# Kernel tuning notes

Hardware: AMD Instinct MI355X
Metric: run time of the kernel (lower is better)

The kernel has to match this reference:

```python
import jax, jax.numpy as jnp
import numpy as np

N_NODES = 50000
N_EDGES = 800000
F_IN, HID, N_CLS = 128, 64, 40


def gcn_conv(x, edge_index, W, b):
    """PyG GCNConv: add self-loops, symmetric normalization, linear, aggregate, bias."""
    n = x.shape[0]
    loop = jnp.arange(n, dtype=edge_index.dtype)
    src = jnp.concatenate([edge_index[0], loop])  # [E+N]
    dst = jnp.concatenate([edge_index[1], loop])  # [E+N]
    deg = jax.ops.segment_sum(jnp.ones_like(dst, dtype=x.dtype), dst, num_segments=n)
    dinv = jnp.where(deg > 0, jax.lax.rsqrt(deg), 0.0)
    norm = dinv[src] * dinv[dst]                   # [E+N]
    h = x @ W                                      # [N, out]
    out = jax.ops.segment_sum(h[src] * norm[:, None], dst, num_segments=n)
    return out + b


def setup_inputs() -> dict:
    key = jax.random.key(0)
    k1, k2, k3, k4 = jax.random.split(key, 4)
    x = jax.random.normal(k1, (N_NODES, F_IN), dtype=jnp.float32)
    edge_index = jax.random.randint(k2, (2, N_EDGES), 0, N_NODES, dtype=jnp.int32)
    W1 = jax.random.normal(k3, (F_IN, HID), dtype=jnp.float32) / np.sqrt(F_IN)
    b1 = jnp.zeros((HID,), dtype=jnp.float32)
    W2 = jax.random.normal(k4, (HID, N_CLS), dtype=jnp.float32) / np.sqrt(HID)
    b2 = jnp.zeros((N_CLS,), dtype=jnp.float32)
    return {"x": x, "edge_index": edge_index, "W1": W1, "b1": b1, "W2": W2, "b2": b2}


def reference(x, edge_index, W1, b1, W2, b2):
    # layer 1: GCNConv -> ReLU -> Dropout(eval = identity)
    h = jax.nn.relu(gcn_conv(x, edge_index, W1, b1))
    # layer 2: GCNConv -> ReLU -> Dropout(eval = identity); return_logits=True
    h = jax.nn.relu(gcn_conv(h, edge_index, W2, b2))
    return h
```

## Files before the change

### kernel.cpp

```cpp
#include <hip/hip_runtime.h>
#include <hip/hip_bf16.h>
#include <hip/hip_fp16.h>


#define N_FEAT_IN 128
#define N_HID 64
#define N_CLS 40
#define CAP 64

__device__ __forceinline__ void h8_acc(uint4 u, float4& a0, float4& a1) {
    __half2* h = (__half2*)&u;
    float2 f0 = __half22float2(h[0]);
    float2 f1 = __half22float2(h[1]);
    float2 f2 = __half22float2(h[2]);
    float2 f3 = __half22float2(h[3]);
    a0.x += f0.x; a0.y += f0.y; a0.z += f1.x; a0.w += f1.y;
    a1.x += f2.x; a1.y += f2.y; a1.z += f3.x; a1.w += f3.y;
}

__device__ __forceinline__ void h8_fma(uint4 u, float w, float4& a0, float4& a1) {
    __half2* h = (__half2*)&u;
    float2 f0 = __half22float2(h[0]);
    float2 f1 = __half22float2(h[1]);
    float2 f2 = __half22float2(h[2]);
    float2 f3 = __half22float2(h[3]);
    a0.x += w * f0.x; a0.y += w * f0.y; a0.z += w * f1.x; a0.w += w * f1.y;
    a1.x += w * f2.x; a1.y += w * f2.y; a1.z += w * f3.x; a1.w += w * f3.y;
}

__device__ __forceinline__ uint4 f8_to_h8(float4 a0, float4 a1) {
    uint4 u;
    ((__half2*)&u)[0] = __floats2half2_rn(a0.x, a0.y);
    ((__half2*)&u)[1] = __floats2half2_rn(a0.z, a0.w);
    ((__half2*)&u)[2] = __floats2half2_rn(a1.x, a1.y);
    ((__half2*)&u)[3] = __floats2half2_rn(a1.z, a1.w);
    return u;
}

__device__ __forceinline__ uint2 f4_to_h4(float4 v) {
    uint2 w;
    *(__half2*)&w.x = __floats2half2_rn(v.x, v.y);
    *(__half2*)&w.y = __floats2half2_rn(v.z, v.w);
    return w;
}

__global__ __launch_bounds__(256) void k_g1c(
    const float* __restrict__ x, const float* __restrict__ W,
    __half* __restrict__ h1u, int n, int gb,
    const int* __restrict__ ei, int* deg, int* __restrict__ rank, int E) {
    __shared__ float Wl[64 * 64];
    __shared__ float Xs[64 * 68];
    int t = threadIdx.x;
    if (blockIdx.x >= gb) {
        int e = (blockIdx.x - gb) * 256 + t;
        if (e < E) {
            int d = ei[E + e];
            rank[e] = atomicAdd(&deg[d], 1);
        }
        return;
    }
    int node0 = blockIdx.x * 64;
    int tn = t & 15;
    int tc = t >> 4;
    float acc[4][4] = {};
    for (int p = 0; p < 2; ++p) {
#pragma unroll
        for (int i = 0; i < 4; ++i) {
            int r = (t >> 4) + 16 * i;
            int c4 = t & 15;
            *(float4*)&Wl[r * 64 + c4 * 4] =
                *(const float4*)&W[(p * 64 + r) * N_HID + c4 * 4];
            int gr = node0 + r;
            float4 v = (gr < n)
                ? *(const float4*)&x[(size_t)gr * N_FEAT_IN + p * 64 + c4 * 4]
                : make_float4(0.f, 0.f, 0.f, 0.f);
            *(float4*)&Xs[r * 68 + c4 * 4] = v;
        }
        __syncthreads();
        for (int k = 0; k < 64; k += 4) {
            float4 xa[4], wb[4];
#pragma unroll
            for (int i = 0; i < 4; ++i)
                xa[i] = *(float4*)&Xs[(tn + 16 * i) * 68 + k];
#pragma unroll
            for (int kk = 0; kk < 4; ++kk)
                wb[kk] = *(float4*)&Wl[(k + kk) * 64 + tc * 4];
#pragma unroll
            for (int kk = 0; kk < 4; ++kk)
#pragma unroll
                for (int i = 0; i < 4; ++i)
#pragma unroll
                    for (int j = 0; j < 4; ++j)
                        acc[i][j] += ((const float*)&xa[i])[kk] * ((const float*)&wb[kk])[j];
        }
        __syncthreads();
    }
#pragma unroll
    for (int i = 0; i < 4; ++i) {
        int gr = node0 + tn + 16 * i;
        if (gr < n) {
            float4 v = make_float4(acc[i][0], acc[i][1], acc[i][2], acc[i][3]);
            *(uint2*)(h1u + (size_t)gr * N_HID + tc * 4) = f4_to_h4(v);
        }
    }
}

__global__ __launch_bounds__(256) void k_scat(
    const int* __restrict__ ei, const int* __restrict__ rank,
    unsigned short* __restrict__ csr, int E) {
    int e = blockIdx.x * blockDim.x + threadIdx.x;
    if (e >= E) return;
    int s = ei[e];
    int d = ei[E + e];
    int r = rank[e];
    if (r < CAP) csr[(d << 6) + r] = (unsigned short)s;
}

template <bool L1>
__global__ __launch_bounds__(256) void k_aggrh(const int* __restrict__ dgi,
                                               const unsigned short* __restrict__ csr,
                                               const __half* __restrict__ hs,
                                               const float* __restrict__ b,
                                               __half* __restrict__ outp, int n) {
    __shared__ int Ss[4][2][32];
    int wv = threadIdx.x >> 6, lane = threadIdx.x & 63;
    int hf = lane >> 5;
    int hl = lane & 31;
    int g = hl >> 3;
    int l8 = hl & 7;
    int node = blockIdx.x * 8 + wv * 2 + hf;
    bool active = node < n;
    float4 a0 = make_float4(0.f, 0.f, 0.f, 0.f);
    float4 a1 = make_float4(0.f, 0.f, 0.f, 0.f);
    int dn = 0;
    if (active) dn = dgi[node];
    int cap = min(dn, CAP);
    float din = active ? 1.0f / sqrtf((float)(dn + 1)) : 0.f;
    if (active && g == 0) {
        uint4 u = *(const uint4*)(hs + ((size_t)node << 6) + l8 * 8);
        if (L1) h8_fma(u, din, a0, a1);
        else    h8_acc(u, a0, a1);
    }
    const int base = node << 6;
    for (int j0 = 0; j0 < cap; j0 += 32) {
        int j = j0 + hl;
        if (j < cap) Ss[wv][hf][hl] = (int)csr[base + j];
        int cnt = min(32, cap - j0);
        int t = 0;
        for (; t + 16 <= cnt; t += 16) {
            int s1 = Ss[wv][hf][t + g];
            int s2 = Ss[wv][hf][t + 4 + g];
            int s3 = Ss[wv][hf][t + 8 + g];
            int s4 = Ss[wv][hf][t + 12 + g];
            uint4 u1 = *(const uint4*)(hs + ((size_t)s1 << 6) + l8 * 8);
            uint4 u2 = *(const uint4*)(hs + ((size_t)s2 << 6) + l8 * 8);
            uint4 u3 = *(const uint4*)(hs + ((size_t)s3 << 6) + l8 * 8);
            uint4 u4 = *(const uint4*)(hs + ((size_t)s4 << 6) + l8 * 8);
            if (L1) {
                int d1 = dgi[s1], d2 = dgi[s2], d3 = dgi[s3], d4 = dgi[s4];
                float w1 = 1.0f / sqrtf((float)(d1 + 1));
                float w2 = 1.0f / sqrtf((float)(d2 + 1));
                float w3 = 1.0f / sqrtf((float)(d3 + 1));
                float w4 = 1.0f / sqrtf((float)(d4 + 1));
                h8_fma(u1, w1, a0, a1);
                h8_fma(u2, w2, a0, a1);
                h8_fma(u3, w3, a0, a1);
                h8_fma(u4, w4, a0, a1);
            } else {
                h8_acc(u1, a0, a1);
                h8_acc(u2, a0, a1);
                h8_acc(u3, a0, a1);
                h8_acc(u4, a0, a1);
            }
        }
        if (t + 8 <= cnt) {
            int s1 = Ss[wv][hf][t + g];
            int s2 = Ss[wv][hf][t + 4 + g];
            uint4 u1 = *(const uint4*)(hs + ((size_t)s1 << 6) + l8 * 8);
            uint4 u2 = *(const uint4*)(hs + ((size_t)s2 << 6) + l8 * 8);
            if (L1) {
                int d1 = dgi[s1], d2 = dgi[s2];
                h8_fma(u1, 1.0f / sqrtf((float)(d1 + 1)), a0, a1);
                h8_fma(u2, 1.0f / sqrtf((float)(d2 + 1)), a0, a1);
            } else {
                h8_acc(u1, a0, a1);
                h8_acc(u2, a0, a1);
            }
            t += 8;
        }
        for (; t < cnt; t += 4) {
            int e = t + g;
            if (e < cnt) {
                int s = Ss[wv][hf][e];
                uint4 u = *(const uint4*)(hs + ((size_t)s << 6) + l8 * 8);
                if (L1) {
                    int dd = dgi[s];
                    h8_fma(u, 1.0f / sqrtf((float)(dd + 1)), a0, a1);
                } else {
                    h8_acc(u, a0, a1);
                }
            }
        }
    }
    a0.x += __shfl_xor(a0.x, 8);  a0.y += __shfl_xor(a0.y, 8);
    a0.z += __shfl_xor(a0.z, 8);  a0.w += __shfl_xor(a0.w, 8);
    a1.x += __shfl_xor(a1.x, 8);  a1.y += __shfl_xor(a1.y, 8);
    a1.z += __shfl_xor(a1.z, 8);  a1.w += __shfl_xor(a1.w, 8);
    a0.x += __shfl_xor(a0.x, 16); a0.y += __shfl_xor(a0.y, 16);
    a0.z += __shfl_xor(a0.z, 16); a0.w += __shfl_xor(a0.w, 16);
    a1.x += __shfl_xor(a1.x, 16); a1.y += __shfl_xor(a1.y, 16);
    a1.z += __shfl_xor(a1.z, 16); a1.w += __shfl_xor(a1.w, 16);
    if (active && g == 0) {
        float4 o0, o1;
        if (L1) {
            float4 b0 = *(const float4*)&b[l8 * 8];
            float4 b1 = *(const float4*)&b[l8 * 8 + 4];
            o0.x = fmaxf(din * a0.x + b0.x, 0.f) * din;
            o0.y = fmaxf(din * a0.y + b0.y, 0.f) * din;
            o0.z = fmaxf(din * a0.z + b0.z, 0.f) * din;
            o0.w = fmaxf(din * a0.w + b0.w, 0.f) * din;
            o1.x = fmaxf(din * a1.x + b1.x, 0.f) * din;
            o1.y = fmaxf(din * a1.y + b1.y, 0.f) * din;
            o1.z = fmaxf(din * a1.z + b1.z, 0.f) * din;
            o1.w = fmaxf(din * a1.w + b1.w, 0.f) * din;
        } else {
            o0 = make_float4(din * a0.x, din * a0.y, din * a0.z, din * a0.w);
            o1 = make_float4(din * a1.x, din * a1.y, din * a1.z, din * a1.w);
        }
        *(uint4*)(outp + ((size_t)node << 6) + l8 * 8) = f8_to_h8(o0, o1);
    }
}

__global__ __launch_bounds__(256, 2) void k_gemm2f(const __half* __restrict__ g2,
                                                   const float* __restrict__ W,
                                                   const float* __restrict__ bias,
                                                   float* __restrict__ out, int n) {
    __shared__ float Wl[N_HID * N_CLS];
    __shared__ float Xs[64 * 68];
    int t = threadIdx.x;
    int node0 = blockIdx.x * 64;
    for (int i = t * 4; i < N_HID * N_CLS; i += 1024)
        *(float4*)&Wl[i] = *(const float4*)&W[i];
#pragma unroll
    for (int q = 0; q < 2; ++q) {
        int idx = q * 256 + t;
        int r = idx >> 3, c8 = idx & 7;
        int gr = node0 + r;
        uint4 u = make_uint4(0u, 0u, 0u, 0u);
        if (gr < n) u = *(const uint4*)(g2 + (size_t)gr * N_HID + c8 * 8);
        __half2* h = (__half2*)&u;
        float2 f0 = __half22float2(h[0]);
        float2 f1 = __half22float2(h[1]);
        float2 f2 = __half22float2(h[2]);
        float2 f3 = __half22float2(h[3]);
        float* xp = &Xs[r * 68 + c8 * 8];
        *(float4*)&xp[0] = make_float4(f0.x, f0.y, f1.x, f1.y);
        *(float4*)&xp[4] = make_float4(f2.x, f2.y, f3.x, f3.y);
    }
    __syncthreads();
    int tn = t & 15;
    int tc = t >> 4;
    if (tc < 10) {
        float acc[4][4] = {};
        for (int k = 0; k < N_HID; k += 4) {
            float4 xa[4], wb[4];
#pragma unroll
            for (int i = 0; i < 4; ++i)
                xa[i] = *(float4*)&Xs[(tn + 16 * i) * 68 + k];
#pragma unroll
            for (int kk = 0; kk < 4; ++kk)
                wb[kk] = *(float4*)&Wl[(k + kk) * N_CLS + tc * 4];
#pragma unroll
            for (int kk = 0; kk < 4; ++kk)
#pragma unroll
                for (int i = 0; i < 4; ++i)
#pragma unroll
                    for (int j = 0; j < 4; ++j)
                        acc[i][j] += ((const float*)&xa[i])[kk] * ((const float*)&wb[kk])[j];
        }
        float4 bv = *(const float4*)&bias[tc * 4];
#pragma unroll
        for (int i = 0; i < 4; ++i) {
            int gr = node0 + tn + 16 * i;
            if (gr < n) {
                float4 v = make_float4(fmaxf(acc[i][0] + bv.x, 0.f),
                                       fmaxf(acc[i][1] + bv.y, 0.f),
                                       fmaxf(acc[i][2] + bv.z, 0.f),
                                       fmaxf(acc[i][3] + bv.w, 0.f));
                *(float4*)&out[(size_t)gr * N_CLS + tc * 4] = v;
            }
        }
    }
}

extern "C" void kernel_launch(void* const* d_in, const int* in_sizes, int n_in,
                              void* d_out, int out_size, void* d_ws, size_t ws_size,
                              hipStream_t stream) {
    const float* x = (const float*)d_in[0];
    const int* ei = (const int*)d_in[1];
    const float* W1 = (const float*)d_in[2];
    const float* b1 = (const float*)d_in[3];
    const float* W2 = (const float*)d_in[4];
    const float* b2 = (const float*)d_in[5];
    float* out = (float*)d_out;

    int n = in_sizes[0] / N_FEAT_IN;
    int E = in_sizes[1] / 2;

    char* ws = (char*)d_ws;
    int*            deg_i = (int*)           (ws + 0);
    int*            rank  = (int*)           (ws + 200704);
    unsigned short* csr   = (unsigned short*)(ws + 3400704);
    __half*         h1u   = (__half*)        (ws + 9800704);
    __half*         out1s = (__half*)        (ws + 16200704);
    __half*         g2h   = h1u;

    int gb = (n + 63) / 64;
    int cb = (E + 255) / 256;

    hipMemsetAsync(deg_i, 0, (size_t)n * sizeof(int), stream);
    k_g1c<<<gb + cb, 256, 0, stream>>>(x, W1, h1u, n, gb, ei, deg_i, rank, E);
    k_scat<<<cb, 256, 0, stream>>>(ei, rank, csr, E);

    k_aggrh<true><<<(n + 7) / 8, 256, 0, stream>>>(deg_i, csr, h1u,
                                                   b1, out1s, n);
    k_aggrh<false><<<(n + 7) / 8, 256, 0, stream>>>(deg_i, csr, out1s,
                                                    nullptr, g2h, n);
    k_gemm2f<<<gb, 256, 0, stream>>>(g2h, W2, b2, out, n);
}
```

Baseline: 104.9 us.

## Prescale layer-1 features by source norm in scatter kernel, drop per-edge degree loads

Layer-1 features are now multiplied by dinv[src] once per node inside the CSR scatter kernel, using extra blocks appended to that launch. The layer-1 aggregation then sums plain rows instead of loading the source degree and computing an rsqrt for every edge. The degree-count blocks in the first kernel also each handle four edges per thread, so fewer blocks are launched. In exchange, the scatter pass reads and writes the whole half-precision feature array once more and rounds it to fp16 a second time.

```diff
diff --git a/kernel.cpp b/kernel.cpp
--- a/kernel.cpp
+++ b/kernel.cpp
@@ -18,16 +18,6 @@
     a1.x += f2.x; a1.y += f2.y; a1.z += f3.x; a1.w += f3.y;
 }
 
-__device__ __forceinline__ void h8_fma(uint4 u, float w, float4& a0, float4& a1) {
-    __half2* h = (__half2*)&u;
-    float2 f0 = __half22float2(h[0]);
-    float2 f1 = __half22float2(h[1]);
-    float2 f2 = __half22float2(h[2]);
-    float2 f3 = __half22float2(h[3]);
-    a0.x += w * f0.x; a0.y += w * f0.y; a0.z += w * f1.x; a0.w += w * f1.y;
-    a1.x += w * f2.x; a1.y += w * f2.y; a1.z += w * f3.x; a1.w += w * f3.y;
-}
-
 __device__ __forceinline__ uint4 f8_to_h8(float4 a0, float4 a1) {
     uint4 u;
     ((__half2*)&u)[0] = __floats2half2_rn(a0.x, a0.y);
@@ -52,10 +42,14 @@
     __shared__ float Xs[64 * 68];
     int t = threadIdx.x;
     if (blockIdx.x >= gb) {
-        int e = (blockIdx.x - gb) * 256 + t;
-        if (e < E) {
-            int d = ei[E + e];
-            rank[e] = atomicAdd(&deg[d], 1);
+        int e0 = (blockIdx.x - gb) * 1024 + t;
+#pragma unroll
+        for (int q = 0; q < 4; ++q) {
+            int e = e0 + q * 256;
+            if (e < E) {
+                int d = ei[E + e];
+                rank[e] = atomicAdd(&deg[d], 1);
+            }
         }
         return;
     }
@@ -107,13 +101,30 @@
 
 __global__ __launch_bounds__(256) void k_scat(
     const int* __restrict__ ei, const int* __restrict__ rank,
-    unsigned short* __restrict__ csr, int E) {
-    int e = blockIdx.x * blockDim.x + threadIdx.x;
-    if (e >= E) return;
-    int s = ei[e];
-    int d = ei[E + e];
-    int r = rank[e];
-    if (r < CAP) csr[(d << 6) + r] = (unsigned short)s;
+    unsigned short* __restrict__ csr, int E, int cb,
+    const int* __restrict__ deg, __half* __restrict__ h1u, int n) {
+    if (blockIdx.x < cb) {
+        int e = blockIdx.x * blockDim.x + threadIdx.x;
+        if (e >= E) return;
+        int s = ei[e];
+        int d = ei[E + e];
+        int r = rank[e];
+        if (r < CAP) csr[(d << 6) + r] = (unsigned short)s;
+        return;
+    }
+    int i = (blockIdx.x - cb) * 256 + threadIdx.x;
+    if (i >= n * 8) return;
+    int node = i >> 3;
+    float din = 1.0f / sqrtf((float)(deg[node] + 1));
+    uint4 u = ((uint4*)h1u)[i];
+    __half2* h = (__half2*)&u;
+    float2 f0 = __half22float2(h[0]);
+    float2 f1 = __half22float2(h[1]);
+    float2 f2 = __half22float2(h[2]);
+    float2 f3 = __half22float2(h[3]);
+    float4 a0 = make_float4(din * f0.x, din * f0.y, din * f1.x, din * f1.y);
+    float4 a1 = make_float4(din * f2.x, din * f2.y, din * f3.x, din * f3.y);
+    ((uint4*)h1u)[i] = f8_to_h8(a0, a1);
 }
 
 template <bool L1>
@@ -138,8 +149,7 @@
     float din = active ? 1.0f / sqrtf((float)(dn + 1)) : 0.f;
     if (active && g == 0) {
         uint4 u = *(const uint4*)(hs + ((size_t)node << 6) + l8 * 8);
-        if (L1) h8_fma(u, din, a0, a1);
-        else    h8_acc(u, a0, a1);
+        h8_acc(u, a0, a1);
     }
     const int base = node << 6;
     for (int j0 = 0; j0 < cap; j0 += 32) {
@@ -156,36 +166,18 @@
             uint4 u2 = *(const uint4*)(hs + ((size_t)s2 << 6) + l8 * 8);
             uint4 u3 = *(const uint4*)(hs + ((size_t)s3 << 6) + l8 * 8);
             uint4 u4 = *(const uint4*)(hs + ((size_t)s4 << 6) + l8 * 8);
-            if (L1) {
-                int d1 = dgi[s1], d2 = dgi[s2], d3 = dgi[s3], d4 = dgi[s4];
-                float w1 = 1.0f / sqrtf((float)(d1 + 1));
-                float w2 = 1.0f / sqrtf((float)(d2 + 1));
-                float w3 = 1.0f / sqrtf((float)(d3 + 1));
-                float w4 = 1.0f / sqrtf((float)(d4 + 1));
-                h8_fma(u1, w1, a0, a1);
-                h8_fma(u2, w2, a0, a1);
-                h8_fma(u3, w3, a0, a1);
-                h8_fma(u4, w4, a0, a1);
-            } else {
-                h8_acc(u1, a0, a1);
-                h8_acc(u2, a0, a1);
-                h8_acc(u3, a0, a1);
-                h8_acc(u4, a0, a1);
-            }
+            h8_acc(u1, a0, a1);
+            h8_acc(u2, a0, a1);
+            h8_acc(u3, a0, a1);
+            h8_acc(u4, a0, a1);
         }
         if (t + 8 <= cnt) {
             int s1 = Ss[wv][hf][t + g];
             int s2 = Ss[wv][hf][t + 4 + g];
             uint4 u1 = *(const uint4*)(hs + ((size_t)s1 << 6) + l8 * 8);
             uint4 u2 = *(const uint4*)(hs + ((size_t)s2 << 6) + l8 * 8);
-            if (L1) {
-                int d1 = dgi[s1], d2 = dgi[s2];
-                h8_fma(u1, 1.0f / sqrtf((float)(d1 + 1)), a0, a1);
-                h8_fma(u2, 1.0f / sqrtf((float)(d2 + 1)), a0, a1);
-            } else {
-                h8_acc(u1, a0, a1);
-                h8_acc(u2, a0, a1);
-            }
+            h8_acc(u1, a0, a1);
+            h8_acc(u2, a0, a1);
             t += 8;
         }
         for (; t < cnt; t += 4) {
@@ -193,12 +185,7 @@
             if (e < cnt) {
                 int s = Ss[wv][hf][e];
                 uint4 u = *(const uint4*)(hs + ((size_t)s << 6) + l8 * 8);
-                if (L1) {
-                    int dd = dgi[s];
-                    h8_fma(u, 1.0f / sqrtf((float)(dd + 1)), a0, a1);
-                } else {
-                    h8_acc(u, a0, a1);
-                }
+                h8_acc(u, a0, a1);
             }
         }
     }
@@ -317,10 +304,12 @@
 
     int gb = (n + 63) / 64;
     int cb = (E + 255) / 256;
+    int cb4 = (E + 1023) / 1024;
+    int sb = (n * 8 + 255) / 256;
 
     hipMemsetAsync(deg_i, 0, (size_t)n * sizeof(int), stream);
-    k_g1c<<<gb + cb, 256, 0, stream>>>(x, W1, h1u, n, gb, ei, deg_i, rank, E);
-    k_scat<<<cb, 256, 0, stream>>>(ei, rank, csr, E);
+    k_g1c<<<gb + cb4, 256, 0, stream>>>(x, W1, h1u, n, gb, ei, deg_i, rank, E);
+    k_scat<<<cb + sb, 256, 0, stream>>>(ei, rank, csr, E, cb, deg_i, h1u, n);
 
     k_aggrh<true><<<(n + 7) / 8, 256, 0, stream>>>(deg_i, csr, h1u,
                                                    b1, out1s, n);
```

After: 104.5 us, median of 2. No clear change (-0.3%).
